# Optimization experiments

Hardware: AMD Instinct MI355X
Metric: run time of the kernel (lower is better)

Reference implementation:

```python
import jax, jax.numpy as jnp
import numpy as np

QMAX = 127.0
QMIN = -128.0
THRESHOLD = 5e-07

def setup_inputs() -> dict:
    key = jax.random.key(0)
    k1, k2, k3 = jax.random.split(key, 3)
    B, S, Din, Dout = 4, 2048, 4096, 4096
    x = jax.random.normal(k1, (B, S, Din), dtype=jnp.float32)
    # Emulate QuantizedLinear.__init__: per-output-channel symmetric int8 weight quant
    w_fp = jax.random.normal(k2, (Dout, Din), dtype=jnp.float32) * 0.02
    w_scale = jnp.clip(jnp.max(jnp.abs(w_fp), axis=1, keepdims=True), THRESHOLD, None) / QMAX  # [Dout,1]
    weight = jnp.round(w_fp / w_scale)  # int8-valued, stored float32, [Dout, Din]
    weight_scale = w_scale.reshape(1, 1, Dout)  # [1,1,Dout]
    bias = jax.random.normal(k3, (Dout,), dtype=jnp.float32) * 0.01
    return {"x": x, "weight": weight, "weight_scale": weight_scale, "bias": bias}

def reference(x, weight, weight_scale, bias):
    # Dynamic per-tensor activation quantization (act_quant=True, no fixed range)
    fp_min = jnp.min(x)
    fp_max = jnp.max(x)
    scale = (fp_max - fp_min) / (QMAX - QMIN)
    zero_point = jnp.clip(jnp.round(QMIN - fp_min / scale), QMIN, QMAX)
    q_input = jnp.round(x / scale + zero_point)  # int8-valued float
    # F.linear(q_input - zp, weight): [B,S,Din] x [Dout,Din]^T -> [B,S,Dout]
    y = jnp.einsum('bsd,od->bso', q_input - zero_point, weight)
    y = y * scale * weight_scale  # dequant epilogue (weight_scale broadcasts [1,1,Dout])
    return y + bias
```

## Files before the change

### kernel.cpp

```cpp
#include <hip/hip_runtime.h>
#include <hip/hip_bf16.h>
#include <stdint.h>

typedef __attribute__((ext_vector_type(4))) int i32x4;

#define K_DIM 4096
#define M_DIM 8192
#define N_DIM 4096

#define BM 256
#define BN 256
#define BKB 128
#define K_TILES (K_DIM / BKB)
#define GITERS (K_TILES / 2)

__device__ __forceinline__ void gload_lds16(const void* g, void* l) {
    __builtin_amdgcn_global_load_lds(
        (__attribute__((address_space(1))) void*)(void*)g,
        (__attribute__((address_space(3))) void*)(void*)l,
        16, 0, 0);
}

__global__ void minmax_kernel(const float* __restrict__ x, long n4,
                              float* __restrict__ partials) {
    const float4* x4 = (const float4*)x;
    float mn = 1e30f, mx = -1e30f;
    long stride = (long)gridDim.x * blockDim.x;
    for (long i = (long)blockIdx.x * blockDim.x + threadIdx.x; i < n4; i += stride) {
        float4 v = x4[i];
        mn = fminf(mn, fminf(fminf(v.x, v.y), fminf(v.z, v.w)));
        mx = fmaxf(mx, fmaxf(fmaxf(v.x, v.y), fmaxf(v.z, v.w)));
    }
    #pragma unroll
    for (int off = 32; off; off >>= 1) {
        mn = fminf(mn, __shfl_down(mn, off));
        mx = fmaxf(mx, __shfl_down(mx, off));
    }
    __shared__ float smn[4], smx[4];
    int wid = threadIdx.x >> 6, lane = threadIdx.x & 63;
    if (lane == 0) { smn[wid] = mn; smx[wid] = mx; }
    __syncthreads();
    if (threadIdx.x == 0) {
        mn = fminf(fminf(smn[0], smn[1]), fminf(smn[2], smn[3]));
        mx = fmaxf(fmaxf(smx[0], smx[1]), fmaxf(smx[2], smx[3]));
        partials[blockIdx.x] = mn;
        partials[1024 + blockIdx.x] = mx;
    }
}

__global__ void finalize_kernel(const float* __restrict__ partials,
                                float* __restrict__ scal) {
    float mn = 1e30f, mx = -1e30f;
    for (int i = threadIdx.x; i < 1024; i += 256) {
        mn = fminf(mn, partials[i]);
        mx = fmaxf(mx, partials[1024 + i]);
    }
    #pragma unroll
    for (int off = 32; off; off >>= 1) {
        mn = fminf(mn, __shfl_down(mn, off));
        mx = fmaxf(mx, __shfl_down(mx, off));
    }
    __shared__ float smn[4], smx[4];
    int wid = threadIdx.x >> 6, lane = threadIdx.x & 63;
    if (lane == 0) { smn[wid] = mn; smx[wid] = mx; }
    __syncthreads();
    if (threadIdx.x == 0) {
        mn = fminf(fminf(smn[0], smn[1]), fminf(smn[2], smn[3]));
        mx = fmaxf(fmaxf(smx[0], smx[1]), fmaxf(smx[2], smx[3]));
        float scale = (mx - mn) / 255.0f;
        float zp = rintf(-128.0f - mn / scale);
        zp = fminf(fmaxf(zp, -128.0f), 127.0f);
        scal[0] = scale;
        scal[1] = zp;
    }
}

__global__ void quantize_kernel(const float* __restrict__ x,
                                const float* __restrict__ scal,
                                uint4* __restrict__ q, long n16) {
    float scale = scal[0];
    float zp = scal[1];
    long stride = (long)gridDim.x * blockDim.x;
    for (long i = (long)blockIdx.x * blockDim.x + threadIdx.x; i < n16; i += stride) {
        const float4* xp = (const float4*)x + i * 4;
        unsigned wrd[4];
        #pragma unroll
        for (int w = 0; w < 4; w++) {
            float4 v = xp[w];
            float e[4] = {v.x, v.y, v.z, v.w};
            unsigned word = 0;
            #pragma unroll
            for (int j = 0; j < 4; j++) {
                float qf = rintf(e[j] / scale + zp);
                qf = fminf(fmaxf(qf, -128.0f), 127.0f);
                int iq = (int)qf;
                word |= ((unsigned)iq & 0xffu) << (8 * j);
            }
            wrd[w] = word;
        }
        uint4 o; o.x = wrd[0]; o.y = wrd[1]; o.z = wrd[2]; o.w = wrd[3];
        q[i] = o;
    }
}

__global__ void convw_kernel(const float* __restrict__ w,
                             signed char* __restrict__ Wq,
                             int* __restrict__ rowsum) {
    int row = blockIdx.x * 4 + (threadIdx.x >> 6);
    int lane = threadIdx.x & 63;
    const float4* src = (const float4*)(w + (long)row * K_DIM);
    uint4* dst = (uint4*)(Wq + (long)row * K_DIM);
    float s = 0.f;
    #pragma unroll
    for (int k = 0; k < 4; k++) {
        int u = k * 64 + lane;
        unsigned wrd[4];
        #pragma unroll
        for (int j = 0; j < 4; j++) {
            float4 v = src[u * 4 + j];
            float e[4] = {v.x, v.y, v.z, v.w};
            unsigned word = 0;
            #pragma unroll
            for (int b = 0; b < 4; b++) {
                int iv = (int)e[b];
                s += e[b];
                word |= ((unsigned)iv & 0xffu) << (8 * b);
            }
            wrd[j] = word;
        }
        uint4 o; o.x = wrd[0]; o.y = wrd[1]; o.z = wrd[2]; o.w = wrd[3];
        dst[u] = o;
    }
    #pragma unroll
    for (int off = 32; off; off >>= 1) s += __shfl_down(s, off);
    if (lane == 0) rowsum[row] = (int)s;
}

__global__ void fold_kernel(const float* __restrict__ scal,
                            const int* __restrict__ rowsum,
                            const float* __restrict__ wscale,
                            const float* __restrict__ bias,
                            float* __restrict__ outscale,
                            float* __restrict__ bias2) {
    int n = blockIdx.x * 256 + threadIdx.x;
    float scale = scal[0], zp = scal[1];
    float os = scale * wscale[n];
    outscale[n] = os;
    bias2[n] = bias[n] - zp * (float)rowsum[n] * os;
}

__global__ __launch_bounds__(512, 2) void gemm_kernel(
    const signed char* __restrict__ A,
    const signed char* __restrict__ W,
    const float* __restrict__ outscale,
    const float* __restrict__ bias2,
    float* __restrict__ C) {
    extern __shared__ char lds[];
    char* As = lds;
    char* Bs = lds + 65536;

    int nwg = gridDim.x;
    int cpx = nwg >> 3;
    int bid = blockIdx.x;
    int wg = (bid & 7) * cpx + (bid >> 3);
    int tm = wg >> 4;
    int tn = wg & 15;
    int m0 = tm * BM, n0 = tn * BN;

    int t = threadIdx.x;
    int wid = t >> 6, lane = t & 63;
    int wr = wid >> 2, wc = wid & 3;
    int lr = lane & 15, lk = lane >> 4;
    int ksw0 = (lk ^ (lr & 7)) * 16;
    int ksw1 = ((4 + lk) ^ (lr & 7)) * 16;

    int R0 = t >> 3;
    int csw = ((t & 7) ^ ((t >> 3) & 7)) * 16;
    const signed char* aSrc = A + (long)(m0 + R0) * K_DIM + csw;
    const signed char* bSrc = W + (long)(n0 + ((R0 >> 5) << 6) + (R0 & 31)) * K_DIM + csw;
    int ldd = t * 16;

#define STAGE_A(BUF, UN, KT) do { \
    const signed char* _s = aSrc + (long)(UN) * 64 * K_DIM + (long)(KT) * BKB; \
    char* _d = As + (BUF) * 32768 + (UN) * 16384 + ldd; \
    gload_lds16(_s, _d); \
    gload_lds16(_s + (long)128 * K_DIM, _d + 8192); } while (0)

#define STAGE_B(BUF, UN, KT) do { \
    const signed char* _s = bSrc + (long)(UN) * 32 * K_DIM + (long)(KT) * BKB; \
    char* _d = Bs + (BUF) * 32768 + (UN) * 16384 + ldd; \
    gload_lds16(_s, _d); \
    gload_lds16(_s + (long)128 * K_DIM, _d + 8192); } while (0)

#define READ_A(BUF, MH) do { \
    const char* _p = As + (BUF) * 32768 + (MH) * 16384 + (wr * 64 + lr) * 128; \
    _Pragma("unroll") \
    for (int _mm = 0; _mm < 4; ++_mm) { \
        a[_mm * 2]     = *(const i32x4*)(_p + _mm * 2048 + ksw0); \
        a[_mm * 2 + 1] = *(const i32x4*)(_p + _mm * 2048 + ksw1); } } while (0)

#define READ_B(BUF, NH, BR) do { \
    const char* _p = Bs + (BUF) * 32768 + (NH) * 16384 + (wc * 32 + lr) * 128; \
    _Pragma("unroll") \
    for (int _nn = 0; _nn < 2; ++_nn) { \
        BR[_nn * 2]     = *(const i32x4*)(_p + _nn * 2048 + ksw0); \
        BR[_nn * 2 + 1] = *(const i32x4*)(_p + _nn * 2048 + ksw1); } } while (0)

#define MFMA_QUAD(MH, NH, BR) do { \
    _Pragma("unroll") \
    for (int _mm = 0; _mm < 4; ++_mm) \
    _Pragma("unroll") \
    for (int _nn = 0; _nn < 2; ++_nn) { \
        acc[(MH) * 4 + _mm][(NH) * 2 + _nn] = __builtin_amdgcn_mfma_i32_16x16x64_i8( \
            a[_mm * 2], BR[_nn * 2], acc[(MH) * 4 + _mm][(NH) * 2 + _nn], 0, 0, 0); \
        acc[(MH) * 4 + _mm][(NH) * 2 + _nn] = __builtin_amdgcn_mfma_i32_16x16x64_i8( \
            a[_mm * 2 + 1], BR[_nn * 2 + 1], acc[(MH) * 4 + _mm][(NH) * 2 + _nn], 0, 0, 0); } } while (0)

#define BAR()   asm volatile("s_barrier" ::: "memory")
#define LGKM0() asm volatile("s_waitcnt lgkmcnt(0)" ::: "memory")
#define LGKM8() asm volatile("s_waitcnt lgkmcnt(8)" ::: "memory")
#define VM6()   asm volatile("s_waitcnt vmcnt(6)" ::: "memory")
#define VM0()   asm volatile("s_waitcnt vmcnt(0)" ::: "memory")
#define PRIO1() __builtin_amdgcn_s_setprio(1)
#define PRIO0() __builtin_amdgcn_s_setprio(0)

    i32x4 acc[8][4];
    #pragma unroll
    for (int i = 0; i < 8; i++)
        #pragma unroll
        for (int j = 0; j < 4; j++)
            acc[i][j] = (i32x4){0, 0, 0, 0};

    i32x4 a[8], b0[4], b1[4];

    STAGE_A(0, 0, 0); STAGE_B(0, 0, 0); STAGE_B(0, 1, 0); STAGE_A(0, 1, 0);
    STAGE_A(1, 0, 1); STAGE_B(1, 0, 1); STAGE_B(1, 1, 1);
    VM6();
    BAR();

    for (int it = 0; it < GITERS; ++it) {
        int t1 = 2 * it + 1;
        int tn0 = 2 * it + 2, tn1 = 2 * it + 3;
        bool st = (it < GITERS - 1);

        READ_A(0, 0);
        READ_B(0, 0, b0);
        STAGE_A(1, 1, t1);
        LGKM8();
        BAR(); LGKM0();
        PRIO1(); MFMA_QUAD(0, 0, b0); PRIO0();
        BAR();

        READ_B(0, 1, b1);
        if (st) STAGE_A(0, 0, tn0);
        BAR(); LGKM0();
        PRIO1(); MFMA_QUAD(0, 1, b1); PRIO0();
        BAR();

        READ_A(0, 1);
        if (st) STAGE_B(0, 0, tn0);
        BAR(); LGKM0();
        PRIO1(); MFMA_QUAD(1, 1, b1); PRIO0();
        BAR();

        if (st) { STAGE_B(0, 1, tn0); VM6(); } else { VM0(); }
        BAR();
        PRIO1(); MFMA_QUAD(1, 0, b0); PRIO0();
        BAR();

        READ_A(1, 0);
        READ_B(1, 0, b0);
        if (st) STAGE_A(0, 1, tn0);
        LGKM8();
        BAR(); LGKM0();
        PRIO1(); MFMA_QUAD(0, 0, b0); PRIO0();
        BAR();

        READ_B(1, 1, b1);
        if (st) STAGE_A(1, 0, tn1);
        BAR(); LGKM0();
        PRIO1(); MFMA_QUAD(0, 1, b1); PRIO0();
        BAR();

        READ_A(1, 1);
        if (st) STAGE_B(1, 0, tn1);
        BAR(); LGKM0();
        PRIO1(); MFMA_QUAD(1, 1, b1); PRIO0();
        BAR();

        if (st) { STAGE_B(1, 1, tn1); VM6(); }
        BAR();
        PRIO1(); MFMA_QUAD(1, 0, b0); PRIO0();
        BAR();
    }

    #pragma unroll
    for (int j = 0; j < 4; j++) {
        int col = n0 + wc * 64 + j * 16 + lr;
        float os = outscale[col];
        float bs = bias2[col];
        #pragma unroll
        for (int i = 0; i < 8; i++) {
            int rbase = m0 + wr * 128 + i * 16 + lk * 4;
            #pragma unroll
            for (int r = 0; r < 4; r++) {
                C[(long)(rbase + r) * N_DIM + col] = (float)acc[i][j][r] * os + bs;
            }
        }
    }
#undef STAGE_A
#undef STAGE_B
#undef READ_A
#undef READ_B
#undef MFMA_QUAD
}

extern "C" void kernel_launch(void* const* d_in, const int* in_sizes, int n_in,
                              void* d_out, int out_size, void* d_ws, size_t ws_size,
                              hipStream_t stream) {
    const float* x      = (const float*)d_in[0];
    const float* weight = (const float*)d_in[1];
    const float* wscale = (const float*)d_in[2];
    const float* bias   = (const float*)d_in[3];
    float* out = (float*)d_out;

    char* ws = (char*)d_ws;
    signed char* Aq = (signed char*)ws;
    signed char* Wq = (signed char*)(ws + (size_t)32 * 1024 * 1024);
    float* partials = (float*)(ws + (size_t)48 * 1024 * 1024);
    float* scal     = partials + 2048;
    int*   rowsum   = (int*)(scal + 16);
    float* outsc    = (float*)(rowsum + 4096);
    float* bias2    = outsc + 4096;

    long n_x = (long)M_DIM * K_DIM;

    minmax_kernel<<<1024, 256, 0, stream>>>(x, n_x / 4, partials);
    finalize_kernel<<<1, 256, 0, stream>>>(partials, scal);
    quantize_kernel<<<2048, 256, 0, stream>>>(x, scal, (uint4*)Aq, n_x / 16);
    convw_kernel<<<1024, 256, 0, stream>>>(weight, Wq, rowsum);
    fold_kernel<<<16, 256, 0, stream>>>(scal, rowsum, wscale, bias, outsc, bias2);

    int lds_bytes = 131072;
    (void)hipFuncSetAttribute((const void*)gemm_kernel,
                              hipFuncAttributeMaxDynamicSharedMemorySize,
                              lds_bytes);
    dim3 grid((M_DIM / BM) * (N_DIM / BN));
    gemm_kernel<<<grid, 512, lds_bytes, stream>>>(Aq, Wq, outsc, bias2, out);
}
```

Baseline: 206.5 us.

## Switch GEMM to 32x32x32 int8 MFMA and merge finalize with fold kernel

The GEMM inner loop now uses 32x32x32 int8 MFMA instructions instead of 16x16x64, with new LDS fragment reads, swizzle offsets, accumulator layout and epilogue row mapping. The larger MFMA tile cuts the number of instructions and the LDS fragment traffic per unit of math. Separately, the finalize and fold kernels are merged into one single-block kernel, and convw is moved earlier so one launch is removed. The risk is in the changed lane-to-row mapping and LDS bank-conflict behaviour of the new swizzle.

```diff
diff --git a/kernel.cpp b/kernel.cpp
--- a/kernel.cpp
+++ b/kernel.cpp
@@ -3,6 +3,7 @@
 #include <stdint.h>
 
 typedef __attribute__((ext_vector_type(4))) int i32x4;
+typedef __attribute__((ext_vector_type(16))) int i32x16;
 
 #define K_DIM 4096
 #define M_DIM 8192
@@ -48,8 +49,46 @@
     }
 }
 
-__global__ void finalize_kernel(const float* __restrict__ partials,
-                                float* __restrict__ scal) {
+__global__ void convw_kernel(const float* __restrict__ w,
+                             signed char* __restrict__ Wq,
+                             int* __restrict__ rowsum) {
+    int row = blockIdx.x * 4 + (threadIdx.x >> 6);
+    int lane = threadIdx.x & 63;
+    const float4* src = (const float4*)(w + (long)row * K_DIM);
+    uint4* dst = (uint4*)(Wq + (long)row * K_DIM);
+    float s = 0.f;
+    #pragma unroll
+    for (int k = 0; k < 4; k++) {
+        int u = k * 64 + lane;
+        unsigned wrd[4];
+        #pragma unroll
+        for (int j = 0; j < 4; j++) {
+            float4 v = src[u * 4 + j];
+            float e[4] = {v.x, v.y, v.z, v.w};
+            unsigned word = 0;
+            #pragma unroll
+            for (int b = 0; b < 4; b++) {
+                int iv = (int)e[b];
+                s += e[b];
+                word |= ((unsigned)iv & 0xffu) << (8 * b);
+            }
+            wrd[j] = word;
+        }
+        uint4 o; o.x = wrd[0]; o.y = wrd[1]; o.z = wrd[2]; o.w = wrd[3];
+        dst[u] = o;
+    }
+    #pragma unroll
+    for (int off = 32; off; off >>= 1) s += __shfl_down(s, off);
+    if (lane == 0) rowsum[row] = (int)s;
+}
+
+__global__ void finalize_fold_kernel(const float* __restrict__ partials,
+                                     const int* __restrict__ rowsum,
+                                     const float* __restrict__ wscale,
+                                     const float* __restrict__ bias,
+                                     float* __restrict__ scal,
+                                     float* __restrict__ outscale,
+                                     float* __restrict__ bias2) {
     float mn = 1e30f, mx = -1e30f;
     for (int i = threadIdx.x; i < 1024; i += 256) {
         mn = fminf(mn, partials[i]);
@@ -61,6 +100,7 @@
         mx = fmaxf(mx, __shfl_down(mx, off));
     }
     __shared__ float smn[4], smx[4];
+    __shared__ float s_scale, s_zp;
     int wid = threadIdx.x >> 6, lane = threadIdx.x & 63;
     if (lane == 0) { smn[wid] = mn; smx[wid] = mx; }
     __syncthreads();
@@ -72,6 +112,14 @@
         zp = fminf(fmaxf(zp, -128.0f), 127.0f);
         scal[0] = scale;
         scal[1] = zp;
+        s_scale = scale; s_zp = zp;
+    }
+    __syncthreads();
+    float scale = s_scale, zp = s_zp;
+    for (int i = threadIdx.x; i < 4096; i += 256) {
+        float os = scale * wscale[i];
+        outscale[i] = os;
+        bias2[i] = bias[i] - zp * (float)rowsum[i] * os;
     }
 }
 
@@ -103,52 +151,6 @@
     }
 }
 
-__global__ void convw_kernel(const float* __restrict__ w,
-                             signed char* __restrict__ Wq,
-                             int* __restrict__ rowsum) {
-    int row = blockIdx.x * 4 + (threadIdx.x >> 6);
-    int lane = threadIdx.x & 63;
-    const float4* src = (const float4*)(w + (long)row * K_DIM);
-    uint4* dst = (uint4*)(Wq + (long)row * K_DIM);
-    float s = 0.f;
-    #pragma unroll
-    for (int k = 0; k < 4; k++) {
-        int u = k * 64 + lane;
-        unsigned wrd[4];
-        #pragma unroll
-        for (int j = 0; j < 4; j++) {
-            float4 v = src[u * 4 + j];
-            float e[4] = {v.x, v.y, v.z, v.w};
-            unsigned word = 0;
-            #pragma unroll
-            for (int b = 0; b < 4; b++) {
-                int iv = (int)e[b];
-                s += e[b];
-                word |= ((unsigned)iv & 0xffu) << (8 * b);
-            }
-            wrd[j] = word;
-        }
-        uint4 o; o.x = wrd[0]; o.y = wrd[1]; o.z = wrd[2]; o.w = wrd[3];
-        dst[u] = o;
-    }
-    #pragma unroll
-    for (int off = 32; off; off >>= 1) s += __shfl_down(s, off);
-    if (lane == 0) rowsum[row] = (int)s;
-}
-
-__global__ void fold_kernel(const float* __restrict__ scal,
-                            const int* __restrict__ rowsum,
-                            const float* __restrict__ wscale,
-                            const float* __restrict__ bias,
-                            float* __restrict__ outscale,
-                            float* __restrict__ bias2) {
-    int n = blockIdx.x * 256 + threadIdx.x;
-    float scale = scal[0], zp = scal[1];
-    float os = scale * wscale[n];
-    outscale[n] = os;
-    bias2[n] = bias[n] - zp * (float)rowsum[n] * os;
-}
-
 __global__ __launch_bounds__(512, 2) void gemm_kernel(
     const signed char* __restrict__ A,
     const signed char* __restrict__ W,
@@ -170,9 +172,12 @@
     int t = threadIdx.x;
     int wid = t >> 6, lane = t & 63;
     int wr = wid >> 2, wc = wid & 3;
-    int lr = lane & 15, lk = lane >> 4;
-    int ksw0 = (lk ^ (lr & 7)) * 16;
-    int ksw1 = ((4 + lk) ^ (lr & 7)) * 16;
+    int l31 = lane & 31, lhi = lane >> 5;
+    int sw = l31 & 7;
+    int sb0 = ((2 * 0 + lhi) ^ sw) * 16;
+    int sb1 = ((2 * 1 + lhi) ^ sw) * 16;
+    int sb2 = ((2 * 2 + lhi) ^ sw) * 16;
+    int sb3 = ((2 * 3 + lhi) ^ sw) * 16;
 
     int R0 = t >> 3;
     int csw = ((t & 7) ^ ((t >> 3) & 7)) * 16;
@@ -192,29 +197,29 @@
     gload_lds16(_s, _d); \
     gload_lds16(_s + (long)128 * K_DIM, _d + 8192); } while (0)
 
-#define READ_A(BUF, MH) do { \
-    const char* _p = As + (BUF) * 32768 + (MH) * 16384 + (wr * 64 + lr) * 128; \
+#define READ_A32(BUF, MH) do { \
+    const char* _pa = As + (BUF) * 32768 + (MH) * 16384 + (wr * 64 + l31) * 128; \
     _Pragma("unroll") \
-    for (int _mm = 0; _mm < 4; ++_mm) { \
-        a[_mm * 2]     = *(const i32x4*)(_p + _mm * 2048 + ksw0); \
-        a[_mm * 2 + 1] = *(const i32x4*)(_p + _mm * 2048 + ksw1); } } while (0)
-
-#define READ_B(BUF, NH, BR) do { \
-    const char* _p = Bs + (BUF) * 32768 + (NH) * 16384 + (wc * 32 + lr) * 128; \
+    for (int _m = 0; _m < 2; ++_m) { \
+        aF[_m * 4 + 0] = *(const i32x4*)(_pa + _m * 4096 + sb0); \
+        aF[_m * 4 + 1] = *(const i32x4*)(_pa + _m * 4096 + sb1); \
+        aF[_m * 4 + 2] = *(const i32x4*)(_pa + _m * 4096 + sb2); \
+        aF[_m * 4 + 3] = *(const i32x4*)(_pa + _m * 4096 + sb3); } } while (0)
+
+#define READ_B32(BUF, NH, BF) do { \
+    const char* _pb = Bs + (BUF) * 32768 + (NH) * 16384 + (wc * 32 + l31) * 128; \
+    BF[0] = *(const i32x4*)(_pb + sb0); \
+    BF[1] = *(const i32x4*)(_pb + sb1); \
+    BF[2] = *(const i32x4*)(_pb + sb2); \
+    BF[3] = *(const i32x4*)(_pb + sb3); } while (0)
+
+#define MFMA_QUAD32(MH, NH, BF) do { \
     _Pragma("unroll") \
-    for (int _nn = 0; _nn < 2; ++_nn) { \
-        BR[_nn * 2]     = *(const i32x4*)(_p + _nn * 2048 + ksw0); \
-        BR[_nn * 2 + 1] = *(const i32x4*)(_p + _nn * 2048 + ksw1); } } while (0)
-
-#define MFMA_QUAD(MH, NH, BR) do { \
+    for (int _m = 0; _m < 2; ++_m) \
     _Pragma("unroll") \
-    for (int _mm = 0; _mm < 4; ++_mm) \
-    _Pragma("unroll") \
-    for (int _nn = 0; _nn < 2; ++_nn) { \
-        acc[(MH) * 4 + _mm][(NH) * 2 + _nn] = __builtin_amdgcn_mfma_i32_16x16x64_i8( \
-            a[_mm * 2], BR[_nn * 2], acc[(MH) * 4 + _mm][(NH) * 2 + _nn], 0, 0, 0); \
-        acc[(MH) * 4 + _mm][(NH) * 2 + _nn] = __builtin_amdgcn_mfma_i32_16x16x64_i8( \
-            a[_mm * 2 + 1], BR[_nn * 2 + 1], acc[(MH) * 4 + _mm][(NH) * 2 + _nn], 0, 0, 0); } } while (0)
+    for (int _s = 0; _s < 4; ++_s) \
+        acc[(MH) * 2 + _m][NH] = __builtin_amdgcn_mfma_i32_32x32x32_i8( \
+            aF[_m * 4 + _s], BF[_s], acc[(MH) * 2 + _m][NH], 0, 0, 0); } while (0)
 
 #define BAR()   asm volatile("s_barrier" ::: "memory")
 #define LGKM0() asm volatile("s_waitcnt lgkmcnt(0)" ::: "memory")
@@ -224,14 +229,14 @@
 #define PRIO1() __builtin_amdgcn_s_setprio(1)
 #define PRIO0() __builtin_amdgcn_s_setprio(0)
 
-    i32x4 acc[8][4];
-    #pragma unroll
-    for (int i = 0; i < 8; i++)
+    i32x16 acc[4][2];
+    #pragma unroll
+    for (int i = 0; i < 4; i++)
         #pragma unroll
-        for (int j = 0; j < 4; j++)
-            acc[i][j] = (i32x4){0, 0, 0, 0};
-
-    i32x4 a[8], b0[4], b1[4];
+        for (int j = 0; j < 2; j++)
+            acc[i][j] = (i32x16){0,0,0,0,0,0,0,0,0,0,0,0,0,0,0,0};
+
+    i32x4 aF[8], b0[4], b1[4];
 
     STAGE_A(0, 0, 0); STAGE_B(0, 0, 0); STAGE_B(0, 1, 0); STAGE_A(0, 1, 0);
     STAGE_A(1, 0, 1); STAGE_B(1, 0, 1); STAGE_B(1, 1, 1);
@@ -243,76 +248,77 @@
         int tn0 = 2 * it + 2, tn1 = 2 * it + 3;
         bool st = (it < GITERS - 1);
 
-        READ_A(0, 0);
-        READ_B(0, 0, b0);
+        READ_A32(0, 0);
+        READ_B32(0, 0, b0);
         STAGE_A(1, 1, t1);
         LGKM8();
         BAR(); LGKM0();
-        PRIO1(); MFMA_QUAD(0, 0, b0); PRIO0();
-        BAR();
-
-        READ_B(0, 1, b1);
+        PRIO1(); MFMA_QUAD32(0, 0, b0); PRIO0();
+        BAR();
+
+        READ_B32(0, 1, b1);
         if (st) STAGE_A(0, 0, tn0);
         BAR(); LGKM0();
-        PRIO1(); MFMA_QUAD(0, 1, b1); PRIO0();
-        BAR();
-
-        READ_A(0, 1);
+        PRIO1(); MFMA_QUAD32(0, 1, b1); PRIO0();
+        BAR();
+
+        READ_A32(0, 1);
         if (st) STAGE_B(0, 0, tn0);
         BAR(); LGKM0();
-        PRIO1(); MFMA_QUAD(1, 1, b1); PRIO0();
+        PRIO1(); MFMA_QUAD32(1, 1, b1); PRIO0();
         BAR();
 
         if (st) { STAGE_B(0, 1, tn0); VM6(); } else { VM0(); }
         BAR();
-        PRIO1(); MFMA_QUAD(1, 0, b0); PRIO0();
-        BAR();
-
-        READ_A(1, 0);
-        READ_B(1, 0, b0);
+        PRIO1(); MFMA_QUAD32(1, 0, b0); PRIO0();
+        BAR();
+
+        READ_A32(1, 0);
+        READ_B32(1, 0, b0);
         if (st) STAGE_A(0, 1, tn0);
         LGKM8();
         BAR(); LGKM0();
-        PRIO1(); MFMA_QUAD(0, 0, b0); PRIO0();
-        BAR();
-
-        READ_B(1, 1, b1);
+        PRIO1(); MFMA_QUAD32(0, 0, b0); PRIO0();
+        BAR();
+
+        READ_B32(1, 1, b1);
         if (st) STAGE_A(1, 0, tn1);
         BAR(); LGKM0();
-        PRIO1(); MFMA_QUAD(0, 1, b1); PRIO0();
-        BAR();
-
-        READ_A(1, 1);
+        PRIO1(); MFMA_QUAD32(0, 1, b1); PRIO0();
+        BAR();
+
+        READ_A32(1, 1);
         if (st) STAGE_B(1, 0, tn1);
         BAR(); LGKM0();
-        PRIO1(); MFMA_QUAD(1, 1, b1); PRIO0();
+        PRIO1(); MFMA_QUAD32(1, 1, b1); PRIO0();
         BAR();
 
         if (st) { STAGE_B(1, 1, tn1); VM6(); }
         BAR();
-        PRIO1(); MFMA_QUAD(1, 0, b0); PRIO0();
-        BAR();
-    }
-
-    #pragma unroll
-    for (int j = 0; j < 4; j++) {
-        int col = n0 + wc * 64 + j * 16 + lr;
+        PRIO1(); MFMA_QUAD32(1, 0, b0); PRIO0();
+        BAR();
+    }
+
+    #pragma unroll
+    for (int nj = 0; nj < 2; nj++) {
+        int col = n0 + wc * 64 + nj * 32 + l31;
         float os = outscale[col];
         float bs = bias2[col];
         #pragma unroll
-        for (int i = 0; i < 8; i++) {
-            int rbase = m0 + wr * 128 + i * 16 + lk * 4;
+        for (int mi = 0; mi < 4; mi++) {
+            int rbase = m0 + wr * 128 + mi * 32 + lhi * 4;
             #pragma unroll
-            for (int r = 0; r < 4; r++) {
-                C[(long)(rbase + r) * N_DIM + col] = (float)acc[i][j][r] * os + bs;
+            for (int r = 0; r < 16; r++) {
+                int row = rbase + (r & 3) + 8 * (r >> 2);
+                C[(long)row * N_DIM + col] = (float)acc[mi][nj][r] * os + bs;
             }
         }
     }
 #undef STAGE_A
 #undef STAGE_B
-#undef READ_A
-#undef READ_B
-#undef MFMA_QUAD
+#undef READ_A32
+#undef READ_B32
+#undef MFMA_QUAD32
 }
 
 extern "C" void kernel_launch(void* const* d_in, const int* in_sizes, int n_in,
@@ -336,10 +342,10 @@
     long n_x = (long)M_DIM * K_DIM;
 
     minmax_kernel<<<1024, 256, 0, stream>>>(x, n_x / 4, partials);
-    finalize_kernel<<<1, 256, 0, stream>>>(partials, scal);
+    convw_kernel<<<1024, 256, 0, stream>>>(weight, Wq, rowsum);
+    finalize_fold_kernel<<<1, 256, 0, stream>>>(partials, rowsum, wscale, bias,
+                                                scal, outsc, bias2);
     quantize_kernel<<<2048, 256, 0, stream>>>(x, scal, (uint4*)Aq, n_x / 16);
-    convw_kernel<<<1024, 256, 0, stream>>>(weight, Wq, rowsum);
-    fold_kernel<<<16, 256, 0, stream>>>(scal, rowsum, wscale, bias, outsc, bias2);
 
     int lds_bytes = 131072;
     (void)hipFuncSetAttribute((const void*)gemm_kernel,
```

Result: slower. 226.3 us (+9.6%).
